# Kernel optimization log

Measured on AMD Instinct MI355X. Metric: run time of the kernel, lower is better.

Reference implementation:

```python
import jax, jax.numpy as jnp
import numpy as np

B, S, D = 2, 2048, 2048
H, KV = 32, 8
HD = D // H          # 64
REP = H // KV        # 4


def setup_inputs() -> dict:
    key = jax.random.key(0)
    ks = jax.random.split(key, 7)
    x = jax.random.normal(ks[0], (B, S, D), dtype=jnp.float32)
    # rotary tables: cos/sin of position*inv_freq, shape (S, HD//2)
    inv_freq = 1.0 / (10000.0 ** (np.arange(0, HD, 2, dtype=np.float32) / HD))
    t = np.arange(S, dtype=np.float32)
    freqs = np.outer(t, inv_freq)
    freqs_cos = jnp.asarray(np.cos(freqs))
    freqs_sin = jnp.asarray(np.sin(freqs))
    sc = 0.02
    wq = jax.random.normal(ks[1], (D, D), dtype=jnp.float32) * sc
    wk = jax.random.normal(ks[2], (KV * HD, D), dtype=jnp.float32) * sc
    wv = jax.random.normal(ks[3], (KV * HD, D), dtype=jnp.float32) * sc
    wo = jax.random.normal(ks[4], (D, D), dtype=jnp.float32) * sc
    return {"x": x, "freqs_cos": freqs_cos, "freqs_sin": freqs_sin,
            "wq": wq, "wk": wk, "wv": wv, "wo": wo}


def _rope(t, cos, sin):
    # t: (B, S, h, HD); interleaved real/imag pairs along last dim
    r = t[..., 0::2]
    i = t[..., 1::2]
    cos = cos[None, :, None, :]
    sin = sin[None, :, None, :]
    out_r = r * cos - i * sin
    out_i = r * sin + i * cos
    return jnp.stack([out_r, out_i], axis=-1).reshape(t.shape)


def reference(x, freqs_cos, freqs_sin, wq, wk, wv, wo):
    b, s, d = x.shape
    xq = jnp.einsum('bsd,ed->bse', x, wq).reshape(b, s, H, HD)
    xk = jnp.einsum('bsd,ed->bse', x, wk).reshape(b, s, KV, HD)
    xv = jnp.einsum('bsd,ed->bse', x, wv).reshape(b, s, KV, HD)
    xq = _rope(xq, freqs_cos, freqs_sin)
    xk = _rope(xk, freqs_cos, freqs_sin)
    # GQA repeat_kv: (B,S,KV,HD) -> (B,S,H,HD)
    xk = jnp.repeat(xk, REP, axis=2)
    xv = jnp.repeat(xv, REP, axis=2)
    # to (B,H,S,HD)
    q = xq.transpose(0, 2, 1, 3)
    k = xk.transpose(0, 2, 1, 3)
    v = xv.transpose(0, 2, 1, 3)
    scores = jnp.einsum('bhqd,bhkd->bhqk', q, k) / jnp.sqrt(jnp.float32(HD))
    causal = jnp.tril(jnp.ones((s, s), dtype=bool))
    scores = jnp.where(causal[None, None], scores, jnp.float32(-1e30))
    probs = jax.nn.softmax(scores, axis=-1)
    out = jnp.einsum('bhqk,bhkd->bhqd', probs, v)
    out = out.transpose(0, 2, 1, 3).reshape(b, s, d)
    return jnp.einsum('bsd,ed->bse', out, wo)
```

## Files before the change

### kernel.cpp

```cpp
#include <hip/hip_runtime.h>
#include <cstdint>
#include <cstddef>

#define S_LEN 2048
#define D_MODEL 2048
#define NH 32
#define NKV 8
#define HD_ 64
#define BATCH 2
#define KVD 512
#define MTOT 4096

typedef float f32x4 __attribute__((ext_vector_type(4)));
typedef short s16x8 __attribute__((ext_vector_type(8)));
typedef unsigned int u32;
typedef unsigned int u32x4 __attribute__((ext_vector_type(4)));

__device__ __forceinline__ unsigned short f2bf(float f) {
  unsigned int u = __builtin_bit_cast(unsigned int, f);
  u = (u + 0x7fffu + ((u >> 16) & 1u)) >> 16;
  return (unsigned short)u;
}
__device__ __forceinline__ float bf2f(unsigned short h) {
  return __builtin_bit_cast(float, ((unsigned int)h) << 16);
}
__device__ __forceinline__ float fexp2(float x) {
#if __has_builtin(__builtin_amdgcn_exp2f)
  return __builtin_amdgcn_exp2f(x);
#else
  return exp2f(x);
#endif
}

__device__ __forceinline__ void gl_lds16(const void* g, void* l) {
  __builtin_amdgcn_global_load_lds((const __attribute__((address_space(1))) u32*)g,
                                   (__attribute__((address_space(3))) u32*)l, 16, 0, 0);
}

__global__ void cvt_kernel(const float* __restrict__ in, unsigned short* __restrict__ out, int n4) {
  int i = blockIdx.x * blockDim.x + threadIdx.x;
  if (i >= n4) return;
  float4 v = reinterpret_cast<const float4*>(in)[i];
  ushort4 o;
  o.x = f2bf(v.x); o.y = f2bf(v.y); o.z = f2bf(v.z); o.w = f2bf(v.w);
  reinterpret_cast<ushort4*>(out)[i] = o;
}

__global__ void cvt4_kernel(const float* __restrict__ a, const float* __restrict__ b,
                            const float* __restrict__ c, const float* __restrict__ d,
                            unsigned short* __restrict__ oa, unsigned short* __restrict__ ob,
                            unsigned short* __restrict__ oc, unsigned short* __restrict__ od,
                            int na4, int nb4, int nc4, int nd4) {
  int j = blockIdx.x * blockDim.x + threadIdx.x;
  const float* src; unsigned short* dst;
  if (j < na4) { src = a; dst = oa; }
  else {
    j -= na4;
    if (j < nb4) { src = b; dst = ob; }
    else {
      j -= nb4;
      if (j < nc4) { src = c; dst = oc; }
      else {
        j -= nc4;
        if (j >= nd4) return;
        src = d; dst = od;
      }
    }
  }
  float4 v = reinterpret_cast<const float4*>(src)[j];
  ushort4 o;
  o.x = f2bf(v.x); o.y = f2bf(v.y); o.z = f2bf(v.z); o.w = f2bf(v.w);
  reinterpret_cast<ushort4*>(dst)[j] = o;
}

__global__ void rope2_kernel(unsigned short* __restrict__ qb, unsigned short* __restrict__ kb,
                             const float* __restrict__ cosb, const float* __restrict__ sinb,
                             int totq, int totk, float qscale) {
  int i = blockIdx.x * blockDim.x + threadIdx.x;
  unsigned short* buf; int nheads; float scale;
  if (i < totq) { buf = qb; nheads = NH; scale = qscale; }
  else {
    i -= totq;
    if (i >= totk) return;
    buf = kb; nheads = NKV; scale = 1.0f;
  }
  int pair = i & 31;
  int rest = i >> 5;
  int s = (rest / nheads) % S_LEN;
  float c = cosb[s * 32 + pair], sn = sinb[s * 32 + pair];
  size_t base = (size_t)rest * HD_ + (size_t)pair * 2;
  float r  = bf2f(buf[base]);
  float im = bf2f(buf[base + 1]);
  buf[base]     = f2bf((r * c - im * sn) * scale);
  buf[base + 1] = f2bf((r * sn + im * c) * scale);
}

__global__ __launch_bounds__(256) void gemm_qkv(const unsigned short* __restrict__ A,
                                                const unsigned short* __restrict__ Wq,
                                                const unsigned short* __restrict__ Wk,
                                                const unsigned short* __restrict__ Wv,
                                                unsigned short* __restrict__ Cq,
                                                unsigned short* __restrict__ Ck,
                                                unsigned short* __restrict__ Cvt,
                                                int M, int K) {
  __shared__ alignas(16) short As[128 * 32];
  __shared__ alignas(16) short Bs[128 * 32];
  int tid = threadIdx.x;
  int lane = tid & 63, wid = tid >> 6;
  int bx = blockIdx.x;
  const unsigned short* W; int n0, mode;
  if (bx < 16)      { W = Wq; n0 = bx * 128;        mode = 0; }
  else if (bx < 20) { W = Wk; n0 = (bx - 16) * 128; mode = 1; }
  else              { W = Wv; n0 = (bx - 20) * 128; mode = 2; }
  int m0 = blockIdx.y * 128;
  int wm = (wid >> 1) * 64, wn = (wid & 1) * 64;
  int lrow = lane & 15, lkk = lane >> 4;
  int srow = lane >> 2;
  int scb  = (lane & 3) * 16;
  f32x4 acc[4][4] = {};

  for (int k0 = 0; k0 < K; k0 += 32) {
    __syncthreads();
#pragma unroll
    for (int i = 0; i < 2; ++i) {
      int c = wid * 2 + i;
      int row = c * 16 + srow;
      const char* ga = (const char*)A + ((size_t)(m0 + row) * K + k0) * 2 + scb;
      gl_lds16(ga, (char*)As + c * 1024);
      const char* gw = (const char*)W + ((size_t)(n0 + row) * K + k0) * 2 + scb;
      gl_lds16(gw, (char*)Bs + c * 1024);
    }
    __syncthreads();
    s16x8 af[4], bfr[4];
#pragma unroll
    for (int mi = 0; mi < 4; ++mi) {
      int row = wm + mi * 16 + lrow;
      af[mi] = *reinterpret_cast<const s16x8*>((const char*)As + row * 64 + lkk * 16);
    }
#pragma unroll
    for (int ni = 0; ni < 4; ++ni) {
      int row = wn + ni * 16 + lrow;
      bfr[ni] = *reinterpret_cast<const s16x8*>((const char*)Bs + row * 64 + lkk * 16);
    }
#pragma unroll
    for (int mi = 0; mi < 4; ++mi)
#pragma unroll
      for (int ni = 0; ni < 4; ++ni)
        acc[mi][ni] = __builtin_amdgcn_mfma_f32_16x16x32_bf16(af[mi], bfr[ni], acc[mi][ni], 0, 0, 0);
  }

  if (mode == 2) {
#pragma unroll
    for (int mi = 0; mi < 4; ++mi)
#pragma unroll
      for (int ni = 0; ni < 4; ++ni) {
        int col = n0 + wn + ni * 16 + lrow;
        int mrow = m0 + wm + mi * 16 + lkk * 4;
        ushort4 o;
        o.x = f2bf(acc[mi][ni][0]); o.y = f2bf(acc[mi][ni][1]);
        o.z = f2bf(acc[mi][ni][2]); o.w = f2bf(acc[mi][ni][3]);
        *reinterpret_cast<ushort4*>(Cvt + (size_t)col * M + mrow) = o;
      }
  } else {
    unsigned short* C = (mode == 0) ? Cq : Ck;
    int N = (mode == 0) ? D_MODEL : KVD;
#pragma unroll
    for (int mi = 0; mi < 4; ++mi)
#pragma unroll
      for (int ni = 0; ni < 4; ++ni)
#pragma unroll
        for (int r = 0; r < 4; ++r) {
          int row = m0 + wm + mi * 16 + lkk * 4 + r;
          int col = n0 + wn + ni * 16 + lrow;
          C[(size_t)row * N + col] = f2bf(acc[mi][ni][r]);
        }
  }
}

__global__ __launch_bounds__(256) void gemm_out(const unsigned short* __restrict__ A,
                                                const unsigned short* __restrict__ W,
                                                float* __restrict__ Cf,
                                                int M, int N, int K) {
  __shared__ alignas(16) short As[128 * 32];
  __shared__ alignas(16) short Bs[128 * 32];
  int tid = threadIdx.x;
  int lane = tid & 63, wid = tid >> 6;
  int m0 = blockIdx.y * 128;
  int n0 = blockIdx.x * 128;
  int wm = (wid >> 1) * 64, wn = (wid & 1) * 64;
  int lrow = lane & 15, lkk = lane >> 4;
  int srow = lane >> 2;
  int scb  = (lane & 3) * 16;
  f32x4 acc[4][4] = {};

  for (int k0 = 0; k0 < K; k0 += 32) {
    __syncthreads();
#pragma unroll
    for (int i = 0; i < 2; ++i) {
      int c = wid * 2 + i;
      int row = c * 16 + srow;
      const char* ga = (const char*)A + ((size_t)(m0 + row) * K + k0) * 2 + scb;
      gl_lds16(ga, (char*)As + c * 1024);
      const char* gw = (const char*)W + ((size_t)(n0 + row) * K + k0) * 2 + scb;
      gl_lds16(gw, (char*)Bs + c * 1024);
    }
    __syncthreads();
    s16x8 af[4], bfr[4];
#pragma unroll
    for (int mi = 0; mi < 4; ++mi) {
      int row = wm + mi * 16 + lrow;
      af[mi] = *reinterpret_cast<const s16x8*>((const char*)As + row * 64 + lkk * 16);
    }
#pragma unroll
    for (int ni = 0; ni < 4; ++ni) {
      int row = wn + ni * 16 + lrow;
      bfr[ni] = *reinterpret_cast<const s16x8*>((const char*)Bs + row * 64 + lkk * 16);
    }
#pragma unroll
    for (int mi = 0; mi < 4; ++mi)
#pragma unroll
      for (int ni = 0; ni < 4; ++ni)
        acc[mi][ni] = __builtin_amdgcn_mfma_f32_16x16x32_bf16(af[mi], bfr[ni], acc[mi][ni], 0, 0, 0);
  }

#pragma unroll
  for (int mi = 0; mi < 4; ++mi)
#pragma unroll
    for (int ni = 0; ni < 4; ++ni)
#pragma unroll
      for (int r = 0; r < 4; ++r) {
        int row = m0 + wm + mi * 16 + lkk * 4 + r;
        int col = n0 + wn + ni * 16 + lrow;
        Cf[(size_t)row * N + col] = acc[mi][ni][r];
      }
}

__global__ __launch_bounds__(512) void attn_kernel(const unsigned short* __restrict__ Q,
                                                   const unsigned short* __restrict__ Kb,
                                                   const unsigned short* __restrict__ Vt,
                                                   unsigned short* __restrict__ O) {
  __shared__ alignas(16) short Ks[2][64 * 64];
  __shared__ alignas(16) short Vs[2][64 * 64];

  int tid = threadIdx.x, lane = tid & 63, wid = tid >> 6;
  int qi = lane & 15, lk = lane >> 4;
  int bh = blockIdx.y;
  int b = bh / NH, h = bh % NH, kvh = h >> 2;
  size_t bS = (size_t)b * S_LEN;
  int srow = tid >> 3;
  int scb  = (tid & 7) * 16;
  int sw0  = (srow & 7) << 4;

  const char* kbG = (const char*)Kb + (bS * KVD + (size_t)kvh * HD_) * 2;
  const char* vtG = (const char*)Vt + ((size_t)(kvh * 64) * MTOT + bS) * 2;

  s16x8 kr, vr;
  auto GLOAD = [&](int kv0) {
    kr = *reinterpret_cast<const s16x8*>(kbG + (size_t)(kv0 + srow) * (KVD * 2) + scb);
    vr = *reinterpret_cast<const s16x8*>(vtG + (size_t)srow * (MTOT * 2) + kv0 * 2 + scb);
  };
  auto SWRITE = [&](int bf) {
    *reinterpret_cast<s16x8*>((char*)Ks[bf] + srow * 128 + (scb ^ sw0)) = kr;
    *reinterpret_cast<s16x8*>((char*)Vs[bf] + srow * 128 + (scb ^ sw0)) = vr;
  };

#pragma unroll 1
  for (int job = 0; job < 2; ++job) {
    int qtile = (job == 0) ? (int)blockIdx.x : 15 - (int)blockIdx.x;
    int q0 = qtile * 128;
    int nt = 2 * qtile + 2;
    int qlmax = q0 + wid * 16 + 15;

    const unsigned short* qptr = Q + (bS + q0 + wid * 16 + qi) * D_MODEL + h * HD_;
    s16x8 qf0 = *reinterpret_cast<const s16x8*>(qptr + lk * 8);
    s16x8 qf1 = *reinterpret_cast<const s16x8*>(qptr + 32 + lk * 8);

    f32x4 o_acc[4] = {};
    float m_run = -3.0e38f, l_run = 0.f;

    GLOAD(0);
    SWRITE(0);
    __syncthreads();
    int cur = 0;

    for (int t = 0; t < nt; ++t) {
      if (t + 1 < nt) GLOAD((t + 1) * 64);

      if (64 * t <= qlmax) {
        const char* kbase = (const char*)Ks[cur];
        const char* vbase = (const char*)Vs[cur];

        f32x4 st[4];
        __builtin_amdgcn_s_setprio(1);
#pragma unroll
        for (int mt = 0; mt < 4; ++mt) {
          int row = mt * 16 + qi;
          int sw = (row & 7) << 4;
          s16x8 ka0 = *reinterpret_cast<const s16x8*>(kbase + row * 128 + ((lk * 16) ^ sw));
          s16x8 ka1 = *reinterpret_cast<const s16x8*>(kbase + row * 128 + ((64 + lk * 16) ^ sw));
          f32x4 a = {};
          a = __builtin_amdgcn_mfma_f32_16x16x32_bf16(ka0, qf0, a, 0, 0, 0);
          a = __builtin_amdgcn_mfma_f32_16x16x32_bf16(ka1, qf1, a, 0, 0, 0);
          st[mt] = a;
        }
        __builtin_amdgcn_s_setprio(0);

        if (t >= nt - 2) {
          int ql = q0 + wid * 16 + qi;
#pragma unroll
          for (int mt = 0; mt < 4; ++mt)
#pragma unroll
            for (int r = 0; r < 4; ++r) {
              int kvg = 64 * t + mt * 16 + 4 * lk + r;
              if (kvg > ql) st[mt][r] = -3.0e38f;
            }
        }

        float pmax = st[0][0];
#pragma unroll
        for (int mt = 0; mt < 4; ++mt)
#pragma unroll
          for (int r = 0; r < 4; ++r) pmax = fmaxf(pmax, st[mt][r]);
        pmax = fmaxf(pmax, __shfl_xor(pmax, 16, 64));
        pmax = fmaxf(pmax, __shfl_xor(pmax, 32, 64));

        if (!__all(pmax <= m_run + 8.0f)) {
          float mnew = fmaxf(m_run, pmax);
          float alpha = fexp2(m_run - mnew);
          m_run = mnew;
          l_run *= alpha;
          float ar[4];
#pragma unroll
          for (int r = 0; r < 4; ++r) ar[r] = __shfl(alpha, 4 * lk + r, 64);
#pragma unroll
          for (int n = 0; n < 4; ++n)
#pragma unroll
            for (int r = 0; r < 4; ++r) o_acc[n][r] *= ar[r];
        }

        float psum = 0.f;
#pragma unroll
        for (int mt = 0; mt < 4; ++mt)
#pragma unroll
          for (int r = 0; r < 4; ++r) {
            float p = fexp2(st[mt][r] - m_run);
            st[mt][r] = p;
            psum += p;
          }
        psum += __shfl_xor(psum, 16, 64);
        psum += __shfl_xor(psum, 32, 64);
        l_run += psum;

        u32 pk[4][2];
#pragma unroll
        for (int mt = 0; mt < 4; ++mt)
#pragma unroll
          for (int w = 0; w < 2; ++w)
            pk[mt][w] = (u32)f2bf(st[mt][2 * w]) | ((u32)f2bf(st[mt][2 * w + 1]) << 16);

        int s0 = qi + 32 * (lk & 1);
        int s2 = s0 + 16;
        bool hiw = lk >= 2;
        s16x8 pa[2];
#pragma unroll
        for (int ks = 0; ks < 2; ++ks) {
          u32 a0 = (u32)__shfl((int)pk[2 * ks][0], s0, 64), b0 = (u32)__shfl((int)pk[2 * ks + 1][0], s0, 64);
          u32 a1 = (u32)__shfl((int)pk[2 * ks][1], s0, 64), b1 = (u32)__shfl((int)pk[2 * ks + 1][1], s0, 64);
          u32 a2 = (u32)__shfl((int)pk[2 * ks][0], s2, 64), b2 = (u32)__shfl((int)pk[2 * ks + 1][0], s2, 64);
          u32 a3 = (u32)__shfl((int)pk[2 * ks][1], s2, 64), b3 = (u32)__shfl((int)pk[2 * ks + 1][1], s2, 64);
          u32x4 wv_;
          wv_[0] = hiw ? b0 : a0; wv_[1] = hiw ? b1 : a1;
          wv_[2] = hiw ? b2 : a2; wv_[3] = hiw ? b3 : a3;
          pa[ks] = __builtin_bit_cast(s16x8, wv_);
        }

        __builtin_amdgcn_s_setprio(1);
#pragma unroll
        for (int n = 0; n < 4; ++n) {
          int vrw = n * 16 + qi;
          int sw = (vrw & 7) << 4;
          s16x8 vb0 = *reinterpret_cast<const s16x8*>(vbase + vrw * 128 + ((lk * 16) ^ sw));
          s16x8 vb1 = *reinterpret_cast<const s16x8*>(vbase + vrw * 128 + ((64 + lk * 16) ^ sw));
          o_acc[n] = __builtin_amdgcn_mfma_f32_16x16x32_bf16(pa[0], vb0, o_acc[n], 0, 0, 0);
          o_acc[n] = __builtin_amdgcn_mfma_f32_16x16x32_bf16(pa[1], vb1, o_acc[n], 0, 0, 0);
        }
        __builtin_amdgcn_s_setprio(0);
      }

      if (t + 1 < nt) SWRITE(cur ^ 1);
      __syncthreads();
      cur ^= 1;
    }

    float linv[4];
#pragma unroll
    for (int r = 0; r < 4; ++r) linv[r] = 1.0f / __shfl(l_run, 4 * lk + r, 64);
#pragma unroll
    for (int n = 0; n < 4; ++n)
#pragma unroll
      for (int r = 0; r < 4; ++r) {
        size_t row = bS + q0 + wid * 16 + 4 * lk + r;
        int col = h * HD_ + n * 16 + qi;
        O[row * D_MODEL + col] = f2bf(o_acc[n][r] * linv[r]);
      }
  }
}

extern "C" void kernel_launch(void* const* d_in, const int* in_sizes, int n_in,
                              void* d_out, int out_size, void* d_ws, size_t ws_size,
                              hipStream_t stream) {
  const float* x  = (const float*)d_in[0];
  const float* fc = (const float*)d_in[1];
  const float* fs = (const float*)d_in[2];
  const float* wq = (const float*)d_in[3];
  const float* wk = (const float*)d_in[4];
  const float* wv = (const float*)d_in[5];
  const float* wo = (const float*)d_in[6];
  float* out = (float*)d_out;

  const size_t nx  = (size_t)BATCH * S_LEN * D_MODEL;
  const size_t nw  = (size_t)D_MODEL * D_MODEL;
  const size_t nwk = (size_t)KVD * D_MODEL;
  const size_t nkv = (size_t)BATCH * S_LEN * KVD;

  char* ws = (char*)d_ws;
  unsigned short* xb  = (unsigned short*)ws;  ws += nx  * 2;
  unsigned short* wqb = (unsigned short*)ws;  ws += nw  * 2;
  unsigned short* wkb = (unsigned short*)ws;  ws += nwk * 2;
  unsigned short* wvb = (unsigned short*)ws;  ws += nwk * 2;
  unsigned short* wob = (unsigned short*)ws;  ws += nw  * 2;
  unsigned short* qb  = (unsigned short*)ws;  ws += nx  * 2;
  unsigned short* kb  = (unsigned short*)ws;  ws += nkv * 2;
  unsigned short* vtb = (unsigned short*)ws;  ws += nkv * 2;
  unsigned short* ab  = (unsigned short*)ws;  ws += nx  * 2;

  cvt_kernel<<<dim3((nx / 4 + 255) / 256), dim3(256), 0, stream>>>(x, xb, nx / 4);
  {
    int na4 = nw / 4, nb4 = nwk / 4, nc4 = nwk / 4, nd4 = nw / 4;
    int tot = na4 + nb4 + nc4 + nd4;
    cvt4_kernel<<<dim3((tot + 255) / 256), dim3(256), 0, stream>>>(wq, wk, wv, wo, wqb, wkb, wvb, wob,
                                                                   na4, nb4, nc4, nd4);
  }

  const int M = BATCH * S_LEN;
  gemm_qkv<<<dim3(24, M / 128), dim3(256), 0, stream>>>(xb, wqb, wkb, wvb, qb, kb, vtb, M, D_MODEL);

  {
    int totq = BATCH * S_LEN * NH * 32;
    int totk = BATCH * S_LEN * NKV * 32;
    rope2_kernel<<<dim3((totq + totk + 255) / 256), dim3(256), 0, stream>>>(qb, kb, fc, fs, totq, totk,
                                                                            0.18033688011112042f);
  }

  attn_kernel<<<dim3(8, BATCH * NH), dim3(512), 0, stream>>>(qb, kb, vtb, ab);

  gemm_out<<<dim3(D_MODEL / 128, M / 128), dim3(256), 0, stream>>>(ab, wob, out, M, D_MODEL, D_MODEL);
}
```

Measured before the change: 336.3 us.

## Fuse RoPE into QKV GEMM epilogue and double query rows per attention wave

RoPE and the Q scale are applied in the QKV GEMM epilogue using a lane-pair shuffle, which removes the separate rope kernel and its extra pass over Q and K. The input conversion for x is merged with the weight conversion into a single launch. The attention kernel moves to 256 threads, with each wave handling two 16-row query groups, so each K/V LDS fragment load is reused across both groups. The cost is higher register pressure and fewer waves per block, which could reduce latency hiding.

```diff
diff --git a/kernel.cpp b/kernel.cpp
--- a/kernel.cpp
+++ b/kernel.cpp
@@ -10,6 +10,7 @@
 #define BATCH 2
 #define KVD 512
 #define MTOT 4096
+#define QSC 0.18033688011112042f
 
 typedef float f32x4 __attribute__((ext_vector_type(4)));
 typedef short s16x8 __attribute__((ext_vector_type(8)));
@@ -37,33 +38,30 @@
                                    (__attribute__((address_space(3))) u32*)l, 16, 0, 0);
 }
 
-__global__ void cvt_kernel(const float* __restrict__ in, unsigned short* __restrict__ out, int n4) {
-  int i = blockIdx.x * blockDim.x + threadIdx.x;
-  if (i >= n4) return;
-  float4 v = reinterpret_cast<const float4*>(in)[i];
-  ushort4 o;
-  o.x = f2bf(v.x); o.y = f2bf(v.y); o.z = f2bf(v.z); o.w = f2bf(v.w);
-  reinterpret_cast<ushort4*>(out)[i] = o;
-}
-
-__global__ void cvt4_kernel(const float* __restrict__ a, const float* __restrict__ b,
-                            const float* __restrict__ c, const float* __restrict__ d,
-                            unsigned short* __restrict__ oa, unsigned short* __restrict__ ob,
-                            unsigned short* __restrict__ oc, unsigned short* __restrict__ od,
-                            int na4, int nb4, int nc4, int nd4) {
+__global__ void cvt5_kernel(const float* __restrict__ x, const float* __restrict__ a,
+                            const float* __restrict__ b, const float* __restrict__ c,
+                            const float* __restrict__ d,
+                            unsigned short* __restrict__ ox, unsigned short* __restrict__ oa,
+                            unsigned short* __restrict__ ob, unsigned short* __restrict__ oc,
+                            unsigned short* __restrict__ od,
+                            int nx4, int na4, int nb4, int nc4, int nd4) {
   int j = blockIdx.x * blockDim.x + threadIdx.x;
   const float* src; unsigned short* dst;
-  if (j < na4) { src = a; dst = oa; }
+  if (j < nx4) { src = x; dst = ox; }
   else {
-    j -= na4;
-    if (j < nb4) { src = b; dst = ob; }
+    j -= nx4;
+    if (j < na4) { src = a; dst = oa; }
     else {
-      j -= nb4;
-      if (j < nc4) { src = c; dst = oc; }
+      j -= na4;
+      if (j < nb4) { src = b; dst = ob; }
       else {
-        j -= nc4;
-        if (j >= nd4) return;
-        src = d; dst = od;
+        j -= nb4;
+        if (j < nc4) { src = c; dst = oc; }
+        else {
+          j -= nc4;
+          if (j >= nd4) return;
+          src = d; dst = od;
+        }
       }
     }
   }
@@ -73,32 +71,12 @@
   reinterpret_cast<ushort4*>(dst)[j] = o;
 }
 
-__global__ void rope2_kernel(unsigned short* __restrict__ qb, unsigned short* __restrict__ kb,
-                             const float* __restrict__ cosb, const float* __restrict__ sinb,
-                             int totq, int totk, float qscale) {
-  int i = blockIdx.x * blockDim.x + threadIdx.x;
-  unsigned short* buf; int nheads; float scale;
-  if (i < totq) { buf = qb; nheads = NH; scale = qscale; }
-  else {
-    i -= totq;
-    if (i >= totk) return;
-    buf = kb; nheads = NKV; scale = 1.0f;
-  }
-  int pair = i & 31;
-  int rest = i >> 5;
-  int s = (rest / nheads) % S_LEN;
-  float c = cosb[s * 32 + pair], sn = sinb[s * 32 + pair];
-  size_t base = (size_t)rest * HD_ + (size_t)pair * 2;
-  float r  = bf2f(buf[base]);
-  float im = bf2f(buf[base + 1]);
-  buf[base]     = f2bf((r * c - im * sn) * scale);
-  buf[base + 1] = f2bf((r * sn + im * c) * scale);
-}
-
 __global__ __launch_bounds__(256) void gemm_qkv(const unsigned short* __restrict__ A,
                                                 const unsigned short* __restrict__ Wq,
                                                 const unsigned short* __restrict__ Wk,
                                                 const unsigned short* __restrict__ Wv,
+                                                const float* __restrict__ cosb,
+                                                const float* __restrict__ sinb,
                                                 unsigned short* __restrict__ Cq,
                                                 unsigned short* __restrict__ Ck,
                                                 unsigned short* __restrict__ Cvt,
@@ -164,16 +142,25 @@
   } else {
     unsigned short* C = (mode == 0) ? Cq : Ck;
     int N = (mode == 0) ? D_MODEL : KVD;
+    float qs = (mode == 0) ? QSC : 1.0f;
 #pragma unroll
     for (int mi = 0; mi < 4; ++mi)
 #pragma unroll
-      for (int ni = 0; ni < 4; ++ni)
+      for (int ni = 0; ni < 4; ++ni) {
+        int col = n0 + wn + ni * 16 + lrow;
+        int pair = (col & 63) >> 1;
+        float sgn = (col & 1) ? 1.0f : -1.0f;
 #pragma unroll
         for (int r = 0; r < 4; ++r) {
           int row = m0 + wm + mi * 16 + lkk * 4 + r;
-          int col = n0 + wn + ni * 16 + lrow;
-          C[(size_t)row * N + col] = f2bf(acc[mi][ni][r]);
-        }
+          int s = row & (S_LEN - 1);
+          float cv = cosb[s * 32 + pair];
+          float sv = sinb[s * 32 + pair];
+          float v = acc[mi][ni][r];
+          float p = __shfl_xor(v, 1, 64);
+          C[(size_t)row * N + col] = f2bf((v * cv + sgn * p * sv) * qs);
+        }
+      }
   }
 }
 
@@ -235,7 +222,7 @@
       }
 }
 
-__global__ __launch_bounds__(512) void attn_kernel(const unsigned short* __restrict__ Q,
+__global__ __launch_bounds__(256) void attn_kernel(const unsigned short* __restrict__ Q,
                                                    const unsigned short* __restrict__ Kb,
                                                    const unsigned short* __restrict__ Vt,
                                                    unsigned short* __restrict__ O) {
@@ -254,14 +241,18 @@
   const char* kbG = (const char*)Kb + (bS * KVD + (size_t)kvh * HD_) * 2;
   const char* vtG = (const char*)Vt + ((size_t)(kvh * 64) * MTOT + bS) * 2;
 
-  s16x8 kr, vr;
+  s16x8 kr0, kr1, vr0, vr1;
   auto GLOAD = [&](int kv0) {
-    kr = *reinterpret_cast<const s16x8*>(kbG + (size_t)(kv0 + srow) * (KVD * 2) + scb);
-    vr = *reinterpret_cast<const s16x8*>(vtG + (size_t)srow * (MTOT * 2) + kv0 * 2 + scb);
+    kr0 = *reinterpret_cast<const s16x8*>(kbG + (size_t)(kv0 + srow) * (KVD * 2) + scb);
+    kr1 = *reinterpret_cast<const s16x8*>(kbG + (size_t)(kv0 + srow + 32) * (KVD * 2) + scb);
+    vr0 = *reinterpret_cast<const s16x8*>(vtG + (size_t)srow * (MTOT * 2) + kv0 * 2 + scb);
+    vr1 = *reinterpret_cast<const s16x8*>(vtG + (size_t)(srow + 32) * (MTOT * 2) + kv0 * 2 + scb);
   };
   auto SWRITE = [&](int bf) {
-    *reinterpret_cast<s16x8*>((char*)Ks[bf] + srow * 128 + (scb ^ sw0)) = kr;
-    *reinterpret_cast<s16x8*>((char*)Vs[bf] + srow * 128 + (scb ^ sw0)) = vr;
+    *reinterpret_cast<s16x8*>((char*)Ks[bf] + srow * 128 + (scb ^ sw0)) = kr0;
+    *reinterpret_cast<s16x8*>((char*)Ks[bf] + (srow + 32) * 128 + (scb ^ sw0)) = kr1;
+    *reinterpret_cast<s16x8*>((char*)Vs[bf] + srow * 128 + (scb ^ sw0)) = vr0;
+    *reinterpret_cast<s16x8*>((char*)Vs[bf] + (srow + 32) * 128 + (scb ^ sw0)) = vr1;
   };
 
 #pragma unroll 1
@@ -269,14 +260,19 @@
     int qtile = (job == 0) ? (int)blockIdx.x : 15 - (int)blockIdx.x;
     int q0 = qtile * 128;
     int nt = 2 * qtile + 2;
-    int qlmax = q0 + wid * 16 + 15;
-
-    const unsigned short* qptr = Q + (bS + q0 + wid * 16 + qi) * D_MODEL + h * HD_;
-    s16x8 qf0 = *reinterpret_cast<const s16x8*>(qptr + lk * 8);
-    s16x8 qf1 = *reinterpret_cast<const s16x8*>(qptr + 32 + lk * 8);
-
-    f32x4 o_acc[4] = {};
-    float m_run = -3.0e38f, l_run = 0.f;
+    int qw = q0 + wid * 32;
+
+    const unsigned short* qp0 = Q + (bS + qw + qi) * D_MODEL + h * HD_;
+    const unsigned short* qp1 = Q + (bS + qw + 16 + qi) * D_MODEL + h * HD_;
+    s16x8 qfa[2], qfb[2];
+    qfa[0] = *reinterpret_cast<const s16x8*>(qp0 + lk * 8);
+    qfb[0] = *reinterpret_cast<const s16x8*>(qp0 + 32 + lk * 8);
+    qfa[1] = *reinterpret_cast<const s16x8*>(qp1 + lk * 8);
+    qfb[1] = *reinterpret_cast<const s16x8*>(qp1 + 32 + lk * 8);
+
+    f32x4 o_acc[2][4] = {};
+    float m_run[2] = {-3.0e38f, -3.0e38f};
+    float l_run[2] = {0.f, 0.f};
 
     GLOAD(0);
     SWRITE(0);
@@ -286,105 +282,125 @@
     for (int t = 0; t < nt; ++t) {
       if (t + 1 < nt) GLOAD((t + 1) * 64);
 
-      if (64 * t <= qlmax) {
+      if (64 * t <= qw + 31) {
         const char* kbase = (const char*)Ks[cur];
         const char* vbase = (const char*)Vs[cur];
 
-        f32x4 st[4];
-        __builtin_amdgcn_s_setprio(1);
+        s16x8 ka0[4], ka1[4];
 #pragma unroll
         for (int mt = 0; mt < 4; ++mt) {
           int row = mt * 16 + qi;
           int sw = (row & 7) << 4;
-          s16x8 ka0 = *reinterpret_cast<const s16x8*>(kbase + row * 128 + ((lk * 16) ^ sw));
-          s16x8 ka1 = *reinterpret_cast<const s16x8*>(kbase + row * 128 + ((64 + lk * 16) ^ sw));
-          f32x4 a = {};
-          a = __builtin_amdgcn_mfma_f32_16x16x32_bf16(ka0, qf0, a, 0, 0, 0);
-          a = __builtin_amdgcn_mfma_f32_16x16x32_bf16(ka1, qf1, a, 0, 0, 0);
-          st[mt] = a;
-        }
+          ka0[mt] = *reinterpret_cast<const s16x8*>(kbase + row * 128 + ((lk * 16) ^ sw));
+          ka1[mt] = *reinterpret_cast<const s16x8*>(kbase + row * 128 + ((64 + lk * 16) ^ sw));
+        }
+
+        f32x4 st[2][4];
+        __builtin_amdgcn_s_setprio(1);
+#pragma unroll
+        for (int g = 0; g < 2; ++g)
+#pragma unroll
+          for (int mt = 0; mt < 4; ++mt) {
+            f32x4 a = {};
+            a = __builtin_amdgcn_mfma_f32_16x16x32_bf16(ka0[mt], qfa[g], a, 0, 0, 0);
+            a = __builtin_amdgcn_mfma_f32_16x16x32_bf16(ka1[mt], qfb[g], a, 0, 0, 0);
+            st[g][mt] = a;
+          }
         __builtin_amdgcn_s_setprio(0);
 
+        s16x8 vb0[4], vb1[4];
+#pragma unroll
+        for (int n = 0; n < 4; ++n) {
+          int vrw = n * 16 + qi;
+          int sw = (vrw & 7) << 4;
+          vb0[n] = *reinterpret_cast<const s16x8*>(vbase + vrw * 128 + ((lk * 16) ^ sw));
+          vb1[n] = *reinterpret_cast<const s16x8*>(vbase + vrw * 128 + ((64 + lk * 16) ^ sw));
+        }
+
         if (t >= nt - 2) {
-          int ql = q0 + wid * 16 + qi;
+#pragma unroll
+          for (int g = 0; g < 2; ++g) {
+            int ql = qw + 16 * g + qi;
+#pragma unroll
+            for (int mt = 0; mt < 4; ++mt)
+#pragma unroll
+              for (int r = 0; r < 4; ++r) {
+                int kvg = 64 * t + mt * 16 + 4 * lk + r;
+                if (kvg > ql) st[g][mt][r] = -3.0e38f;
+              }
+          }
+        }
+
+        u32 pk[2][4][2];
+#pragma unroll
+        for (int g = 0; g < 2; ++g) {
+          float pmax = st[g][0][0];
 #pragma unroll
           for (int mt = 0; mt < 4; ++mt)
 #pragma unroll
+            for (int r = 0; r < 4; ++r) pmax = fmaxf(pmax, st[g][mt][r]);
+          pmax = fmaxf(pmax, __shfl_xor(pmax, 16, 64));
+          pmax = fmaxf(pmax, __shfl_xor(pmax, 32, 64));
+
+          if (!__all(pmax <= m_run[g] + 8.0f)) {
+            float mnew = fmaxf(m_run[g], pmax);
+            float alpha = fexp2(m_run[g] - mnew);
+            m_run[g] = mnew;
+            l_run[g] *= alpha;
+            float ar[4];
+#pragma unroll
+            for (int r = 0; r < 4; ++r) ar[r] = __shfl(alpha, 4 * lk + r, 64);
+#pragma unroll
+            for (int n = 0; n < 4; ++n)
+#pragma unroll
+              for (int r = 0; r < 4; ++r) o_acc[g][n][r] *= ar[r];
+          }
+
+          float psum = 0.f;
+#pragma unroll
+          for (int mt = 0; mt < 4; ++mt)
+#pragma unroll
             for (int r = 0; r < 4; ++r) {
-              int kvg = 64 * t + mt * 16 + 4 * lk + r;
-              if (kvg > ql) st[mt][r] = -3.0e38f;
+              float p = fexp2(st[g][mt][r] - m_run[g]);
+              st[g][mt][r] = p;
+              psum += p;
             }
-        }
-
-        float pmax = st[0][0];
-#pragma unroll
-        for (int mt = 0; mt < 4; ++mt)
-#pragma unroll
-          for (int r = 0; r < 4; ++r) pmax = fmaxf(pmax, st[mt][r]);
-        pmax = fmaxf(pmax, __shfl_xor(pmax, 16, 64));
-        pmax = fmaxf(pmax, __shfl_xor(pmax, 32, 64));
-
-        if (!__all(pmax <= m_run + 8.0f)) {
-          float mnew = fmaxf(m_run, pmax);
-          float alpha = fexp2(m_run - mnew);
-          m_run = mnew;
-          l_run *= alpha;
-          float ar[4];
-#pragma unroll
-          for (int r = 0; r < 4; ++r) ar[r] = __shfl(alpha, 4 * lk + r, 64);
-#pragma unroll
-          for (int n = 0; n < 4; ++n)
-#pragma unroll
-            for (int r = 0; r < 4; ++r) o_acc[n][r] *= ar[r];
-        }
-
-        float psum = 0.f;
-#pragma unroll
-        for (int mt = 0; mt < 4; ++mt)
-#pragma unroll
-          for (int r = 0; r < 4; ++r) {
-            float p = fexp2(st[mt][r] - m_run);
-            st[mt][r] = p;
-            psum += p;
-          }
-        psum += __shfl_xor(psum, 16, 64);
-        psum += __shfl_xor(psum, 32, 64);
-        l_run += psum;
-
-        u32 pk[4][2];
-#pragma unroll
-        for (int mt = 0; mt < 4; ++mt)
-#pragma unroll
-          for (int w = 0; w < 2; ++w)
-            pk[mt][w] = (u32)f2bf(st[mt][2 * w]) | ((u32)f2bf(st[mt][2 * w + 1]) << 16);
+          psum += __shfl_xor(psum, 16, 64);
+          psum += __shfl_xor(psum, 32, 64);
+          l_run[g] += psum;
+
+#pragma unroll
+          for (int mt = 0; mt < 4; ++mt)
+#pragma unroll
+            for (int w = 0; w < 2; ++w)
+              pk[g][mt][w] = (u32)f2bf(st[g][mt][2 * w]) | ((u32)f2bf(st[g][mt][2 * w + 1]) << 16);
+        }
 
         int s0 = qi + 32 * (lk & 1);
         int s2 = s0 + 16;
         bool hiw = lk >= 2;
-        s16x8 pa[2];
-#pragma unroll
-        for (int ks = 0; ks < 2; ++ks) {
-          u32 a0 = (u32)__shfl((int)pk[2 * ks][0], s0, 64), b0 = (u32)__shfl((int)pk[2 * ks + 1][0], s0, 64);
-          u32 a1 = (u32)__shfl((int)pk[2 * ks][1], s0, 64), b1 = (u32)__shfl((int)pk[2 * ks + 1][1], s0, 64);
-          u32 a2 = (u32)__shfl((int)pk[2 * ks][0], s2, 64), b2 = (u32)__shfl((int)pk[2 * ks + 1][0], s2, 64);
-          u32 a3 = (u32)__shfl((int)pk[2 * ks][1], s2, 64), b3 = (u32)__shfl((int)pk[2 * ks + 1][1], s2, 64);
-          u32x4 wv_;
-          wv_[0] = hiw ? b0 : a0; wv_[1] = hiw ? b1 : a1;
-          wv_[2] = hiw ? b2 : a2; wv_[3] = hiw ? b3 : a3;
-          pa[ks] = __builtin_bit_cast(s16x8, wv_);
-        }
-
-        __builtin_amdgcn_s_setprio(1);
-#pragma unroll
-        for (int n = 0; n < 4; ++n) {
-          int vrw = n * 16 + qi;
-          int sw = (vrw & 7) << 4;
-          s16x8 vb0 = *reinterpret_cast<const s16x8*>(vbase + vrw * 128 + ((lk * 16) ^ sw));
-          s16x8 vb1 = *reinterpret_cast<const s16x8*>(vbase + vrw * 128 + ((64 + lk * 16) ^ sw));
-          o_acc[n] = __builtin_amdgcn_mfma_f32_16x16x32_bf16(pa[0], vb0, o_acc[n], 0, 0, 0);
-          o_acc[n] = __builtin_amdgcn_mfma_f32_16x16x32_bf16(pa[1], vb1, o_acc[n], 0, 0, 0);
-        }
-        __builtin_amdgcn_s_setprio(0);
+#pragma unroll
+        for (int g = 0; g < 2; ++g) {
+          s16x8 pa[2];
+#pragma unroll
+          for (int ks = 0; ks < 2; ++ks) {
+            u32 a0 = (u32)__shfl((int)pk[g][2 * ks][0], s0, 64), b0 = (u32)__shfl((int)pk[g][2 * ks + 1][0], s0, 64);
+            u32 a1 = (u32)__shfl((int)pk[g][2 * ks][1], s0, 64), b1 = (u32)__shfl((int)pk[g][2 * ks + 1][1], s0, 64);
+            u32 a2 = (u32)__shfl((int)pk[g][2 * ks][0], s2, 64), b2 = (u32)__shfl((int)pk[g][2 * ks + 1][0], s2, 64);
+            u32 a3 = (u32)__shfl((int)pk[g][2 * ks][1], s2, 64), b3 = (u32)__shfl((int)pk[g][2 * ks + 1][1], s2, 64);
+            u32x4 wv_;
+            wv_[0] = hiw ? b0 : a0; wv_[1] = hiw ? b1 : a1;
+            wv_[2] = hiw ? b2 : a2; wv_[3] = hiw ? b3 : a3;
+            pa[ks] = __builtin_bit_cast(s16x8, wv_);
+          }
+          __builtin_amdgcn_s_setprio(1);
+#pragma unroll
+          for (int n = 0; n < 4; ++n) {
+            o_acc[g][n] = __builtin_amdgcn_mfma_f32_16x16x32_bf16(pa[0], vb0[n], o_acc[g][n], 0, 0, 0);
+            o_acc[g][n] = __builtin_amdgcn_mfma_f32_16x16x32_bf16(pa[1], vb1[n], o_acc[g][n], 0, 0, 0);
+          }
+          __builtin_amdgcn_s_setprio(0);
+        }
       }
 
       if (t + 1 < nt) SWRITE(cur ^ 1);
@@ -392,17 +408,20 @@
       cur ^= 1;
     }
 
-    float linv[4];
-#pragma unroll
-    for (int r = 0; r < 4; ++r) linv[r] = 1.0f / __shfl(l_run, 4 * lk + r, 64);
-#pragma unroll
-    for (int n = 0; n < 4; ++n)
-#pragma unroll
-      for (int r = 0; r < 4; ++r) {
-        size_t row = bS + q0 + wid * 16 + 4 * lk + r;
-        int col = h * HD_ + n * 16 + qi;
-        O[row * D_MODEL + col] = f2bf(o_acc[n][r] * linv[r]);
-      }
+#pragma unroll
+    for (int g = 0; g < 2; ++g) {
+      float linv[4];
+#pragma unroll
+      for (int r = 0; r < 4; ++r) linv[r] = 1.0f / __shfl(l_run[g], 4 * lk + r, 64);
+#pragma unroll
+      for (int n = 0; n < 4; ++n)
+#pragma unroll
+        for (int r = 0; r < 4; ++r) {
+          size_t row = bS + qw + 16 * g + 4 * lk + r;
+          int col = h * HD_ + n * 16 + qi;
+          O[row * D_MODEL + col] = f2bf(o_acc[g][n][r] * linv[r]);
+        }
+    }
   }
 }
 
@@ -434,25 +453,18 @@
   unsigned short* vtb = (unsigned short*)ws;  ws += nkv * 2;
   unsigned short* ab  = (unsigned short*)ws;  ws += nx  * 2;
 
-  cvt_kernel<<<dim3((nx / 4 + 255) / 256), dim3(256), 0, stream>>>(x, xb, nx / 4);
   {
-    int na4 = nw / 4, nb4 = nwk / 4, nc4 = nwk / 4, nd4 = nw / 4;
-    int tot = na4 + nb4 + nc4 + nd4;
-    cvt4_kernel<<<dim3((tot + 255) / 256), dim3(256), 0, stream>>>(wq, wk, wv, wo, wqb, wkb, wvb, wob,
-                                                                   na4, nb4, nc4, nd4);
+    int nx4 = nx / 4, na4 = nw / 4, nb4 = nwk / 4, nc4 = nwk / 4, nd4 = nw / 4;
+    int tot = nx4 + na4 + nb4 + nc4 + nd4;
+    cvt5_kernel<<<dim3((tot + 255) / 256), dim3(256), 0, stream>>>(x, wq, wk, wv, wo,
+                                                                   xb, wqb, wkb, wvb, wob,
+                                                                   nx4, na4, nb4, nc4, nd4);
   }
 
   const int M = BATCH * S_LEN;
-  gemm_qkv<<<dim3(24, M / 128), dim3(256), 0, stream>>>(xb, wqb, wkb, wvb, qb, kb, vtb, M, D_MODEL);
-
-  {
-    int totq = BATCH * S_LEN * NH * 32;
-    int totk = BATCH * S_LEN * NKV * 32;
-    rope2_kernel<<<dim3((totq + totk + 255) / 256), dim3(256), 0, stream>>>(qb, kb, fc, fs, totq, totk,
-                                                                            0.18033688011112042f);
-  }
-
-  attn_kernel<<<dim3(8, BATCH * NH), dim3(512), 0, stream>>>(qb, kb, vtb, ab);
+  gemm_qkv<<<dim3(24, M / 128), dim3(256), 0, stream>>>(xb, wqb, wkb, wvb, fc, fs, qb, kb, vtb, M, D_MODEL);
+
+  attn_kernel<<<dim3(8, BATCH * NH), dim3(256), 0, stream>>>(qb, kb, vtb, ab);
 
   gemm_out<<<dim3(D_MODEL / 128, M / 128), dim3(256), 0, stream>>>(ab, wob, out, M, D_MODEL, D_MODEL);
 }
```

After: 408.5 us. 21.5% more time.

## Fuse RoPE into QKV GEMM epilogue, merge conversions, remap blocks per XCD

Applied to the files above, without the earlier changes.

Applies rotary embedding and the Q scale in the QKV GEMM epilogue, using a lane shuffle to fetch the paired element, so the separate rope kernel and its extra read and write of Q/K go away. The x and weight fp32-to-bf16 conversions are merged into a single launch. Both GEMMs switch to a 1D grid with an XCD-aware block remapping so that blocks sharing A rows land on the same XCD for L2 reuse. The trade-off is extra cos/sin global loads in the epilogue.

```diff
diff --git a/kernel.cpp b/kernel.cpp
--- a/kernel.cpp
+++ b/kernel.cpp
@@ -10,6 +10,7 @@
 #define BATCH 2
 #define KVD 512
 #define MTOT 4096
+#define QSC 0.18033688011112042f
 
 typedef float f32x4 __attribute__((ext_vector_type(4)));
 typedef short s16x8 __attribute__((ext_vector_type(8)));
@@ -37,33 +38,30 @@
                                    (__attribute__((address_space(3))) u32*)l, 16, 0, 0);
 }
 
-__global__ void cvt_kernel(const float* __restrict__ in, unsigned short* __restrict__ out, int n4) {
-  int i = blockIdx.x * blockDim.x + threadIdx.x;
-  if (i >= n4) return;
-  float4 v = reinterpret_cast<const float4*>(in)[i];
-  ushort4 o;
-  o.x = f2bf(v.x); o.y = f2bf(v.y); o.z = f2bf(v.z); o.w = f2bf(v.w);
-  reinterpret_cast<ushort4*>(out)[i] = o;
-}
-
-__global__ void cvt4_kernel(const float* __restrict__ a, const float* __restrict__ b,
-                            const float* __restrict__ c, const float* __restrict__ d,
-                            unsigned short* __restrict__ oa, unsigned short* __restrict__ ob,
-                            unsigned short* __restrict__ oc, unsigned short* __restrict__ od,
-                            int na4, int nb4, int nc4, int nd4) {
+__global__ void cvt5_kernel(const float* __restrict__ x, const float* __restrict__ a,
+                            const float* __restrict__ b, const float* __restrict__ c,
+                            const float* __restrict__ d,
+                            unsigned short* __restrict__ ox, unsigned short* __restrict__ oa,
+                            unsigned short* __restrict__ ob, unsigned short* __restrict__ oc,
+                            unsigned short* __restrict__ od,
+                            int nx4, int na4, int nb4, int nc4, int nd4) {
   int j = blockIdx.x * blockDim.x + threadIdx.x;
   const float* src; unsigned short* dst;
-  if (j < na4) { src = a; dst = oa; }
+  if (j < nx4) { src = x; dst = ox; }
   else {
-    j -= na4;
-    if (j < nb4) { src = b; dst = ob; }
+    j -= nx4;
+    if (j < na4) { src = a; dst = oa; }
     else {
-      j -= nb4;
-      if (j < nc4) { src = c; dst = oc; }
+      j -= na4;
+      if (j < nb4) { src = b; dst = ob; }
       else {
-        j -= nc4;
-        if (j >= nd4) return;
-        src = d; dst = od;
+        j -= nb4;
+        if (j < nc4) { src = c; dst = oc; }
+        else {
+          j -= nc4;
+          if (j >= nd4) return;
+          src = d; dst = od;
+        }
       }
     }
   }
@@ -73,32 +71,12 @@
   reinterpret_cast<ushort4*>(dst)[j] = o;
 }
 
-__global__ void rope2_kernel(unsigned short* __restrict__ qb, unsigned short* __restrict__ kb,
-                             const float* __restrict__ cosb, const float* __restrict__ sinb,
-                             int totq, int totk, float qscale) {
-  int i = blockIdx.x * blockDim.x + threadIdx.x;
-  unsigned short* buf; int nheads; float scale;
-  if (i < totq) { buf = qb; nheads = NH; scale = qscale; }
-  else {
-    i -= totq;
-    if (i >= totk) return;
-    buf = kb; nheads = NKV; scale = 1.0f;
-  }
-  int pair = i & 31;
-  int rest = i >> 5;
-  int s = (rest / nheads) % S_LEN;
-  float c = cosb[s * 32 + pair], sn = sinb[s * 32 + pair];
-  size_t base = (size_t)rest * HD_ + (size_t)pair * 2;
-  float r  = bf2f(buf[base]);
-  float im = bf2f(buf[base + 1]);
-  buf[base]     = f2bf((r * c - im * sn) * scale);
-  buf[base + 1] = f2bf((r * sn + im * c) * scale);
-}
-
 __global__ __launch_bounds__(256) void gemm_qkv(const unsigned short* __restrict__ A,
                                                 const unsigned short* __restrict__ Wq,
                                                 const unsigned short* __restrict__ Wk,
                                                 const unsigned short* __restrict__ Wv,
+                                                const float* __restrict__ cosb,
+                                                const float* __restrict__ sinb,
                                                 unsigned short* __restrict__ Cq,
                                                 unsigned short* __restrict__ Ck,
                                                 unsigned short* __restrict__ Cvt,
@@ -107,12 +85,15 @@
   __shared__ alignas(16) short Bs[128 * 32];
   int tid = threadIdx.x;
   int lane = tid & 63, wid = tid >> 6;
-  int bx = blockIdx.x;
+  int bid = blockIdx.x;
+  int xcd = bid & 7, ii = bid >> 3;
+  int mrow = xcd * 4 + ii / 24;
+  int nb = ii % 24;
   const unsigned short* W; int n0, mode;
-  if (bx < 16)      { W = Wq; n0 = bx * 128;        mode = 0; }
-  else if (bx < 20) { W = Wk; n0 = (bx - 16) * 128; mode = 1; }
-  else              { W = Wv; n0 = (bx - 20) * 128; mode = 2; }
-  int m0 = blockIdx.y * 128;
+  if (nb < 16)      { W = Wq; n0 = nb * 128;        mode = 0; }
+  else if (nb < 20) { W = Wk; n0 = (nb - 16) * 128; mode = 1; }
+  else              { W = Wv; n0 = (nb - 20) * 128; mode = 2; }
+  int m0 = mrow * 128;
   int wm = (wid >> 1) * 64, wn = (wid & 1) * 64;
   int lrow = lane & 15, lkk = lane >> 4;
   int srow = lane >> 2;
@@ -155,25 +136,34 @@
 #pragma unroll
       for (int ni = 0; ni < 4; ++ni) {
         int col = n0 + wn + ni * 16 + lrow;
-        int mrow = m0 + wm + mi * 16 + lkk * 4;
+        int mr = m0 + wm + mi * 16 + lkk * 4;
         ushort4 o;
         o.x = f2bf(acc[mi][ni][0]); o.y = f2bf(acc[mi][ni][1]);
         o.z = f2bf(acc[mi][ni][2]); o.w = f2bf(acc[mi][ni][3]);
-        *reinterpret_cast<ushort4*>(Cvt + (size_t)col * M + mrow) = o;
+        *reinterpret_cast<ushort4*>(Cvt + (size_t)col * M + mr) = o;
       }
   } else {
     unsigned short* C = (mode == 0) ? Cq : Ck;
     int N = (mode == 0) ? D_MODEL : KVD;
+    float qs = (mode == 0) ? QSC : 1.0f;
 #pragma unroll
     for (int mi = 0; mi < 4; ++mi)
 #pragma unroll
-      for (int ni = 0; ni < 4; ++ni)
+      for (int ni = 0; ni < 4; ++ni) {
+        int col = n0 + wn + ni * 16 + lrow;
+        int pair = (col & 63) >> 1;
+        float sgn = (col & 1) ? 1.0f : -1.0f;
 #pragma unroll
         for (int r = 0; r < 4; ++r) {
           int row = m0 + wm + mi * 16 + lkk * 4 + r;
-          int col = n0 + wn + ni * 16 + lrow;
-          C[(size_t)row * N + col] = f2bf(acc[mi][ni][r]);
-        }
+          int s = row & (S_LEN - 1);
+          float cv = cosb[s * 32 + pair];
+          float sv = sinb[s * 32 + pair];
+          float v = acc[mi][ni][r];
+          float p = __shfl_xor(v, 1, 64);
+          C[(size_t)row * N + col] = f2bf((v * cv + sgn * p * sv) * qs);
+        }
+      }
   }
 }
 
@@ -185,8 +175,10 @@
   __shared__ alignas(16) short Bs[128 * 32];
   int tid = threadIdx.x;
   int lane = tid & 63, wid = tid >> 6;
-  int m0 = blockIdx.y * 128;
-  int n0 = blockIdx.x * 128;
+  int bid = blockIdx.x;
+  int xcd = bid & 7, ii = bid >> 3;
+  int m0 = (xcd * 4 + ii / 16) * 128;
+  int n0 = (ii % 16) * 128;
   int wm = (wid >> 1) * 64, wn = (wid & 1) * 64;
   int lrow = lane & 15, lkk = lane >> 4;
   int srow = lane >> 2;
@@ -434,25 +426,18 @@
   unsigned short* vtb = (unsigned short*)ws;  ws += nkv * 2;
   unsigned short* ab  = (unsigned short*)ws;  ws += nx  * 2;
 
-  cvt_kernel<<<dim3((nx / 4 + 255) / 256), dim3(256), 0, stream>>>(x, xb, nx / 4);
   {
-    int na4 = nw / 4, nb4 = nwk / 4, nc4 = nwk / 4, nd4 = nw / 4;
-    int tot = na4 + nb4 + nc4 + nd4;
-    cvt4_kernel<<<dim3((tot + 255) / 256), dim3(256), 0, stream>>>(wq, wk, wv, wo, wqb, wkb, wvb, wob,
-                                                                   na4, nb4, nc4, nd4);
+    int nx4 = nx / 4, na4 = nw / 4, nb4 = nwk / 4, nc4 = nwk / 4, nd4 = nw / 4;
+    int tot = nx4 + na4 + nb4 + nc4 + nd4;
+    cvt5_kernel<<<dim3((tot + 255) / 256), dim3(256), 0, stream>>>(x, wq, wk, wv, wo,
+                                                                   xb, wqb, wkb, wvb, wob,
+                                                                   nx4, na4, nb4, nc4, nd4);
   }
 
   const int M = BATCH * S_LEN;
-  gemm_qkv<<<dim3(24, M / 128), dim3(256), 0, stream>>>(xb, wqb, wkb, wvb, qb, kb, vtb, M, D_MODEL);
-
-  {
-    int totq = BATCH * S_LEN * NH * 32;
-    int totk = BATCH * S_LEN * NKV * 32;
-    rope2_kernel<<<dim3((totq + totk + 255) / 256), dim3(256), 0, stream>>>(qb, kb, fc, fs, totq, totk,
-                                                                            0.18033688011112042f);
-  }
+  gemm_qkv<<<dim3(768), dim3(256), 0, stream>>>(xb, wqb, wkb, wvb, fc, fs, qb, kb, vtb, M, D_MODEL);
 
   attn_kernel<<<dim3(8, BATCH * NH), dim3(512), 0, stream>>>(qb, kb, vtb, ab);
 
-  gemm_out<<<dim3(D_MODEL / 128, M / 128), dim3(256), 0, stream>>>(ab, wob, out, M, D_MODEL, D_MODEL);
-}
+  gemm_out<<<dim3(512), dim3(256), 0, stream>>>(ab, wob, out, M, D_MODEL, D_MODEL);
+}
```

New measurement: 350.1 us. 1.04x slower.
